# Kernel tuning notes

Measured on AMD Instinct MI355X. Metric: run time of the kernel, lower is better.

Reference implementation:

```python
import jax, jax.numpy as jnp
import numpy as np

TOP_K = 2


def setup_inputs() -> dict:
    key = jax.random.key(0)
    k0, k1, k2, k3, k4 = jax.random.split(key, 5)
    B, S, H, I, E = 4, 2048, 1024, 2816, 8
    s_h = 1.0 / np.sqrt(H)
    s_i = 1.0 / np.sqrt(I)
    return {
        "x": jax.random.normal(k0, (B, S, H), jnp.float32),
        # nn.Linear weights are stored as [out_features, in_features]
        "w_router": jax.random.normal(k1, (E, H), jnp.float32) * s_h,   # gate: H -> E
        "w_gate": jax.random.normal(k2, (E, I, H), jnp.float32) * s_h,  # per-expert gate_proj
        "w_up": jax.random.normal(k3, (E, I, H), jnp.float32) * s_h,    # per-expert up_proj
        "w_down": jax.random.normal(k4, (E, H, I), jnp.float32) * s_i,  # per-expert down_proj
    }


def reference(x, w_router, w_gate, w_up, w_down):
    B, S, H = x.shape
    E = w_router.shape[0]
    xf = x.reshape(-1, H)                      # [T, H], T = B*S

    # --- Router: softmax over experts, top-k, renormalize weights ---
    logits = jnp.einsum("th,eh->te", xf, w_router)        # [T, E]
    probs = jax.nn.softmax(logits, axis=-1)
    topw, topi = jax.lax.top_k(probs, TOP_K)              # [T, k]
    topw = topw / jnp.sum(topw, axis=-1, keepdims=True)

    # Per-token combine weight for each expert: sum_k w[t,k] * 1[idx[t,k]==e]
    onehot = (topi[..., None] == jnp.arange(E)).astype(x.dtype)  # [T, k, E]
    combine = jnp.einsum("tk,tke->te", topw, onehot)             # [T, E]

    # --- Experts: SwiGLU MLP per expert on all tokens, masked combine ---
    # (masked-dense in the original == gather-compute mathematically,
    # since silu(0)*0 = 0 and the projections have no bias)
    gate = jax.nn.silu(jnp.einsum("th,eih->eti", xf, w_gate))    # [E, T, I]
    up = jnp.einsum("th,eih->eti", xf, w_up)                     # [E, T, I]
    down = jnp.einsum("eti,ehi->eth", gate * up, w_down)         # [E, T, H]

    out = jnp.einsum("eth,te->th", down, combine)                # [T, H]
    return out.reshape(B, S, H)
```

## Files before the change

kernel.cpp:

```cpp
#include <hip/hip_runtime.h>

#define TT 8192
#define HD 1024
#define ID 2816
#define NE 8
#define NID2 (2*ID)

typedef __attribute__((ext_vector_type(8))) short short8;
typedef __attribute__((ext_vector_type(4))) float f32x4;

#define WS_TOP2I 0
#define WS_TOP2W 65536
#define WS_CNT   131072
#define WS_OFF   131136
#define WS_CUR   131200
#define WS_TMAP  131328
#define WS_SLOTW 196864
#define WS_T2S   262400
#define WS_XB    1048576ULL
#define WS_WGU   (WS_XB  + 16777216ULL)
#define WS_WDB   (WS_WGU + 92274688ULL)
#define WS_ACT   (WS_WDB + 46137344ULL)

__device__ __forceinline__ unsigned int pack_bf2(float lo, float hi) {
  unsigned int ul = __builtin_bit_cast(unsigned int, lo) + 0x8000u;
  unsigned int uh = __builtin_bit_cast(unsigned int, hi) + 0x8000u;
  return (uh & 0xffff0000u) | (ul >> 16);
}

__device__ __forceinline__ unsigned short f2bf(float f) {
  unsigned int u = __builtin_bit_cast(unsigned int, f);
  return (unsigned short)((u + 0x8000u) >> 16);
}

__device__ __forceinline__ void gload16(const void* g, void* l) {
  __builtin_amdgcn_global_load_lds(
      (const __attribute__((address_space(1))) unsigned int*)g,
      (__attribute__((address_space(3))) unsigned int*)l, 16, 0, 0);
}

__global__ __launch_bounds__(256) void router_kernel(
    const float* __restrict__ x, const float* __restrict__ wr,
    int* __restrict__ top2i, float* __restrict__ top2w,
    unsigned short* __restrict__ xb)
{
  int tid  = threadIdx.x;
  int lane = tid & 63;
  int t    = blockIdx.x * 4 + (tid >> 6);

  const float4* xp = (const float4*)(x + (size_t)t * HD + lane * 16);
  float4 xv[4];
  #pragma unroll
  for (int j = 0; j < 4; ++j) xv[j] = xp[j];

  uint4 v0, v1;
  v0.x = pack_bf2(xv[0].x, xv[0].y); v0.y = pack_bf2(xv[0].z, xv[0].w);
  v0.z = pack_bf2(xv[1].x, xv[1].y); v0.w = pack_bf2(xv[1].z, xv[1].w);
  v1.x = pack_bf2(xv[2].x, xv[2].y); v1.y = pack_bf2(xv[2].z, xv[2].w);
  v1.z = pack_bf2(xv[3].x, xv[3].y); v1.w = pack_bf2(xv[3].z, xv[3].w);
  uint4* xrow = (uint4*)(xb + (size_t)t * HD + lane * 16);
  xrow[0] = v0; xrow[1] = v1;

  float acc[NE];
  #pragma unroll
  for (int e = 0; e < NE; ++e) {
    const float4* wp = (const float4*)(wr + (size_t)e * HD + lane * 16);
    float s = 0.f;
    #pragma unroll
    for (int j = 0; j < 4; ++j) {
      float4 w = wp[j];
      s += xv[j].x * w.x + xv[j].y * w.y + xv[j].z * w.z + xv[j].w * w.w;
    }
    acc[e] = s;
  }
  #pragma unroll
  for (int d = 1; d < 64; d <<= 1) {
    #pragma unroll
    for (int e = 0; e < NE; ++e) acc[e] += __shfl_xor(acc[e], d, 64);
  }
  int   i0 = 0; float m0 = acc[0];
  #pragma unroll
  for (int e = 1; e < NE; ++e) if (acc[e] > m0) { m0 = acc[e]; i0 = e; }
  int   i1 = -1; float m1 = -3.4e38f;
  #pragma unroll
  for (int e = 0; e < NE; ++e) if (e != i0 && acc[e] > m1) { m1 = acc[e]; i1 = e; }

  float e1 = __expf(m1 - m0);
  float w0 = 1.f / (1.f + e1);
  float w1 = e1 * w0;

  if (lane == 0) {
    top2i[2 * t] = i0;  top2i[2 * t + 1] = i1;
    top2w[2 * t] = w0;  top2w[2 * t + 1] = w1;
  }
}

__global__ __launch_bounds__(256) void count_scan_kernel(
    const int* __restrict__ top2i,
    int* __restrict__ counts, int* __restrict__ offsets, int* __restrict__ cursors)
{
  __shared__ int s_cnt[NE];
  int tid = threadIdx.x;
  if (tid < NE) s_cnt[tid] = 0;
  __syncthreads();

  int c0=0,c1=0,c2=0,c3=0,c4=0,c5=0,c6=0,c7=0;
  for (int t = tid; t < TT; t += 256) {
    int e0 = top2i[2 * t], e1 = top2i[2 * t + 1];
    c0 += __popcll(__ballot(e0 == 0)) + __popcll(__ballot(e1 == 0));
    c1 += __popcll(__ballot(e0 == 1)) + __popcll(__ballot(e1 == 1));
    c2 += __popcll(__ballot(e0 == 2)) + __popcll(__ballot(e1 == 2));
    c3 += __popcll(__ballot(e0 == 3)) + __popcll(__ballot(e1 == 3));
    c4 += __popcll(__ballot(e0 == 4)) + __popcll(__ballot(e1 == 4));
    c5 += __popcll(__ballot(e0 == 5)) + __popcll(__ballot(e1 == 5));
    c6 += __popcll(__ballot(e0 == 6)) + __popcll(__ballot(e1 == 6));
    c7 += __popcll(__ballot(e0 == 7)) + __popcll(__ballot(e1 == 7));
  }
  if ((tid & 63) == 0) {
    atomicAdd(&s_cnt[0], c0); atomicAdd(&s_cnt[1], c1);
    atomicAdd(&s_cnt[2], c2); atomicAdd(&s_cnt[3], c3);
    atomicAdd(&s_cnt[4], c4); atomicAdd(&s_cnt[5], c5);
    atomicAdd(&s_cnt[6], c6); atomicAdd(&s_cnt[7], c7);
  }
  __syncthreads();
  if (tid == 0) {
    int run = 0;
    #pragma unroll
    for (int e = 0; e < NE; ++e) {
      counts[e] = s_cnt[e]; offsets[e] = run; cursors[e] = run; run += s_cnt[e];
    }
    offsets[NE] = run;
  }
}

__global__ __launch_bounds__(256) void place_kernel(
    const int* __restrict__ top2i, const float* __restrict__ top2w,
    int* __restrict__ cursors,
    int* __restrict__ token_map, float* __restrict__ slot_w, int* __restrict__ tok2slot)
{
  int tid  = threadIdx.x;
  int lane = tid & 63;
  int t    = blockIdx.x * 256 + tid;

  #pragma unroll
  for (int k = 0; k < 2; ++k) {
    int   e = top2i[2 * t + k];
    float w = top2w[2 * t + k];
    #pragma unroll
    for (int ee = 0; ee < NE; ++ee) {
      unsigned long long m = __ballot(e == ee);
      if (e == ee) {
        int leader = __ffsll((long long)m) - 1;
        int pre    = __popcll(m & ((1ull << lane) - 1ull));
        int base   = 0;
        if (lane == leader) base = atomicAdd(&cursors[ee], (int)__popcll(m));
        base = __shfl(base, leader, 64);
        token_map[base + pre] = t;
        slot_w[base + pre]    = w;
        tok2slot[2 * t + k]   = base + pre;
      }
    }
  }
}

__global__ __launch_bounds__(256) void cvt_wgu_kernel(
    const float* __restrict__ wg, const float* __restrict__ wu,
    unsigned short* __restrict__ wgu)
{
  int e    = blockIdx.y;
  int idx  = blockIdx.x * 256 + threadIdx.x;
  int col8 = idx & 127;
  int rr   = idx >> 7;
  int blk  = rr >> 7;
  int win  = rr & 127;
  const float* srow = (win < 64)
      ? wg + ((size_t)e * ID + blk * 64 + win) * HD
      : wu + ((size_t)e * ID + blk * 64 + (win - 64)) * HD;
  const float4* p = (const float4*)(srow + col8 * 8);
  float4 a = p[0], b = p[1];
  uint4 v;
  v.x = pack_bf2(a.x, a.y); v.y = pack_bf2(a.z, a.w);
  v.z = pack_bf2(b.x, b.y); v.w = pack_bf2(b.z, b.w);
  *(uint4*)(wgu + ((size_t)e * NID2 + rr) * HD + col8 * 8) = v;
}

__global__ __launch_bounds__(256) void cvt_bf16_kernel(
    const float* __restrict__ in, unsigned short* __restrict__ out, int n8)
{
  int i = blockIdx.x * 256 + threadIdx.x;
  if (i >= n8) return;
  const float4* p = (const float4*)(in + (size_t)i * 8);
  float4 a = p[0], b = p[1];
  uint4 v;
  v.x = pack_bf2(a.x, a.y); v.y = pack_bf2(a.z, a.w);
  v.z = pack_bf2(b.x, b.y); v.w = pack_bf2(b.z, b.w);
  ((uint4*)out)[i] = v;
}


#define STG(kt) { \
    size_t k1 = (size_t)((kt) * 64); \
    char* db = ldsc + (unsigned)tid * 16; \
    _Pragma("unroll") for (int c = 0; c < 4; ++c) { \
      gload16(aS[c] + k1, db + c * 4096); \
      gload16(bS[c] + k1, db + 16384 + c * 4096); } }

#define CMP() { \
    const char* sa = ldsc; \
    const char* sb = ldsc + 16384; \
    _Pragma("unroll") for (int kk = 0; kk < 2; ++kk) { \
      int kb = kk * 64 + kq; \
      short8 af[4], bfr[4]; \
      _Pragma("unroll") for (int n = 0; n < 4; ++n) \
        bfr[n] = *(const short8*)(sb + (wcn * 64 + n * 16 + arow) * 128 + (kb ^ rxor)); \
      _Pragma("unroll") for (int m = 0; m < 4; ++m) \
        af[m] = *(const short8*)(sa + (wr * 64 + m * 16 + arow) * 128 + (kb ^ rxor)); \
      __builtin_amdgcn_s_setprio(1); \
      _Pragma("unroll") for (int m = 0; m < 4; ++m) \
        _Pragma("unroll") for (int n = 0; n < 4; ++n) \
          acc[m][n] = __builtin_amdgcn_mfma_f32_16x16x32_bf16(af[m], bfr[n], acc[m][n], 0, 0, 0); \
      __builtin_amdgcn_s_setprio(0); \
    } }

#define KLOOP(NT) { \
    for (int kt = 0; kt < (NT); ++kt) { \
      if (kt) __syncthreads(); \
      STG(kt); \
      __syncthreads(); \
      CMP(); \
    } }

#define XCD_DECODE(NX, NY) \
  int nwg  = (NX) * (NY) * NE; \
  int flat = blockIdx.x + (NX) * (blockIdx.y + (NY) * blockIdx.z); \
  int qq   = nwg >> 3; \
  int wg   = (flat & 7) * qq + (flat >> 3); \
  int bx   = wg % (NX); \
  int rem  = wg / (NX); \
  int y    = rem % (NY); \
  int e    = rem / (NY);

__global__ __launch_bounds__(256, 2) void gemm1_fast(
    const unsigned short* __restrict__ xb, const unsigned short* __restrict__ wgu,
    const int* __restrict__ counts, const int* __restrict__ offsets,
    const int* __restrict__ token_map, unsigned short* __restrict__ act)
{
  __shared__ __align__(16) char smem[32768];
  char* ldsc = smem;

  XCD_DECODE(16, 44)
  int cnt = counts[e];
  int off = offsets[e];

  int tid  = threadIdx.x;
  int lane = tid & 63;
  int w    = tid >> 6;
  int wr   = w >> 1;
  int wcn  = w & 1;

  int sr8  = tid >> 3;
  int colE = (((tid & 7) ^ (sr8 & 7)) << 3);
  int rxor = (lane & 7) << 4;
  int arow = lane & 15;
  int kq   = (lane >> 4) << 4;
  int prow = (lane >> 4) << 2;

  for (int t0 = bx * 128; t0 < cnt; t0 += 2048) {
    const unsigned short* aS[4];
    const unsigned short* bS[4];
    #pragma unroll
    for (int c = 0; c < 4; ++c) {
      int rowA = t0 + c * 32 + sr8;
      int slot = off + (rowA < cnt ? rowA : cnt - 1);
      aS[c] = xb  + (size_t)token_map[slot] * HD + colE;
      bS[c] = wgu + ((size_t)e * NID2 + (size_t)y * 128 + c * 32 + sr8) * HD + colE;
    }

    f32x4 zf = {0.f, 0.f, 0.f, 0.f};
    f32x4 acc[4][4];
    #pragma unroll
    for (int m = 0; m < 4; ++m)
      #pragma unroll
      for (int n = 0; n < 4; ++n) acc[m][n] = zf;

    KLOOP(HD / 64);

    __syncthreads();
    float* xch = (float*)smem;
    if (wcn == 1) {
      float* base = xch + wr * 4096;
      #pragma unroll
      for (int m = 0; m < 4; ++m)
        #pragma unroll
        for (int n = 0; n < 4; ++n)
          #pragma unroll
          for (int r = 0; r < 4; ++r)
            base[(m * 16 + prow + r) * 64 + n * 16 + arow] = acc[m][n][r];
    }
    __syncthreads();
    if (wcn == 0) {
      const float* base = xch + wr * 4096;
      #pragma unroll
      for (int m = 0; m < 4; ++m) {
        #pragma unroll
        for (int r = 0; r < 4; ++r) {
          int row = wr * 64 + m * 16 + prow + r;
          int tr2 = t0 + row;
          if (tr2 >= cnt) continue;
          size_t ob = (size_t)(off + tr2) * ID + (size_t)y * 64 + arow;
          #pragma unroll
          for (int n = 0; n < 4; ++n) {
            float g = acc[m][n][r];
            float u = base[(m * 16 + prow + r) * 64 + n * 16 + arow];
            float h = g * u / (1.f + __expf(-g));
            act[ob + n * 16] = f2bf(h);
          }
        }
      }
    }
    __syncthreads();
  }
}

__global__ __launch_bounds__(256, 2) void gemm2_fast(
    const unsigned short* __restrict__ act, const unsigned short* __restrict__ wdb,
    const int* __restrict__ counts, const int* __restrict__ offsets,
    float* __restrict__ down)
{
  __shared__ __align__(16) char smem[32768];
  char* ldsc = smem;

  XCD_DECODE(16, 8)
  int cnt = counts[e];
  int off = offsets[e];

  int tid  = threadIdx.x;
  int lane = tid & 63;
  int w    = tid >> 6;
  int wr   = w >> 1;
  int wcn  = w & 1;

  int sr8  = tid >> 3;
  int colE = (((tid & 7) ^ (sr8 & 7)) << 3);
  int rxor = (lane & 7) << 4;
  int arow = lane & 15;
  int kq   = (lane >> 4) << 4;
  int prow = (lane >> 4) << 2;

  for (int t0 = bx * 128; t0 < cnt; t0 += 2048) {
    const unsigned short* aS[4];
    const unsigned short* bS[4];
    #pragma unroll
    for (int c = 0; c < 4; ++c) {
      int rowA = t0 + c * 32 + sr8;
      int slot = off + (rowA < cnt ? rowA : cnt - 1);
      aS[c] = act + (size_t)slot * ID + colE;
      bS[c] = wdb + ((size_t)e * HD + (size_t)y * 128 + c * 32 + sr8) * ID + colE;
    }

    f32x4 zf = {0.f, 0.f, 0.f, 0.f};
    f32x4 acc[4][4];
    #pragma unroll
    for (int m = 0; m < 4; ++m)
      #pragma unroll
      for (int n = 0; n < 4; ++n) acc[m][n] = zf;

    KLOOP(ID / 64);

    #pragma unroll
    for (int m = 0; m < 4; ++m) {
      #pragma unroll
      for (int r = 0; r < 4; ++r) {
        int row = wr * 64 + m * 16 + prow + r;
        int tr2 = t0 + row;
        if (tr2 >= cnt) continue;
        float* ob = down + (size_t)(off + tr2) * HD + (size_t)y * 128 + wcn * 64 + arow;
        #pragma unroll
        for (int n = 0; n < 4; ++n)
          ob[n * 16] = acc[m][n][r];
      }
    }
    __syncthreads();
  }
}

__global__ __launch_bounds__(256) void combine_kernel(
    const float* __restrict__ down, const float* __restrict__ slot_w,
    const int* __restrict__ tok2slot, float* __restrict__ out)
{
  int t   = blockIdx.x;
  int tid = threadIdx.x;
  int s0  = tok2slot[2 * t], s1 = tok2slot[2 * t + 1];
  float w0 = slot_w[s0], w1 = slot_w[s1];
  const float4* d0 = (const float4*)(down + (size_t)s0 * HD) + tid;
  const float4* d1 = (const float4*)(down + (size_t)s1 * HD) + tid;
  float4 a = *d0, b = *d1;
  float4 o;
  o.x = w0 * a.x + w1 * b.x;  o.y = w0 * a.y + w1 * b.y;
  o.z = w0 * a.z + w1 * b.z;  o.w = w0 * a.w + w1 * b.w;
  ((float4*)(out + (size_t)t * HD))[tid] = o;
}

extern "C" void kernel_launch(void* const* d_in, const int* in_sizes, int n_in,
                              void* d_out, int out_size, void* d_ws, size_t ws_size,
                              hipStream_t stream) {
  const float* x        = (const float*)d_in[0];
  const float* w_router = (const float*)d_in[1];
  const float* w_gate   = (const float*)d_in[2];
  const float* w_up     = (const float*)d_in[3];
  const float* w_down   = (const float*)d_in[4];

  char* ws = (char*)d_ws;
  int*   top2i    = (int*)(ws + WS_TOP2I);
  float* top2w    = (float*)(ws + WS_TOP2W);
  int*   counts   = (int*)(ws + WS_CNT);
  int*   offsets  = (int*)(ws + WS_OFF);
  int*   cursors  = (int*)(ws + WS_CUR);
  int*   tmap     = (int*)(ws + WS_TMAP);
  float* slotw    = (float*)(ws + WS_SLOTW);
  int*   tok2slot = (int*)(ws + WS_T2S);
  unsigned short* xb  = (unsigned short*)(ws + WS_XB);
  unsigned short* wgu = (unsigned short*)(ws + WS_WGU);
  unsigned short* wdb = (unsigned short*)(ws + WS_WDB);
  unsigned short* act = (unsigned short*)(ws + WS_ACT);
  float*          down = (float*)(ws + WS_WGU);

  router_kernel<<<TT / 4, 256, 0, stream>>>(x, w_router, top2i, top2w, xb);
  count_scan_kernel<<<1, 256, 0, stream>>>(top2i, counts, offsets, cursors);
  place_kernel<<<TT / 256, 256, 0, stream>>>(top2i, top2w, cursors, tmap, slotw, tok2slot);
  cvt_wgu_kernel<<<dim3(2816, NE), 256, 0, stream>>>(w_gate, w_up, wgu);
  cvt_bf16_kernel<<<11264, 256, 0, stream>>>(w_down, wdb, NE * HD * ID / 8);

  gemm1_fast<<<dim3(16, 44, NE), 256, 0, stream>>>(xb, wgu, counts, offsets, tmap, act);
  gemm2_fast<<<dim3(16, 8, NE), 256, 0, stream>>>(act, wdb, counts, offsets, down);
  combine_kernel<<<TT, 256, 0, stream>>>(down, slotw, tok2slot, (float*)d_out);
}
```

Measured before the change: 593.0 us.

## Interleave gate/up rows at 16-row granularity and enlarge down-proj GEMM tile

The fused gate/up weight is now interleaved in 16-row chunks, so each wave holds matching gate and up columns in its own accumulators. This removes the LDS exchange and extra barriers in the gemm1 SwiGLU epilogue. gemm2 moves to 512-thread blocks with a 256x256 tile, 128 KB of double-buffered dynamic LDS and 8x4 MFMA tiles per wave, to raise arithmetic intensity. The risks are higher register pressure, lower occupancy, and fewer blocks across the grid.

```diff
diff --git a/kernel.cpp b/kernel.cpp
--- a/kernel.cpp
+++ b/kernel.cpp
@@ -171,11 +171,11 @@
   int idx  = blockIdx.x * 256 + threadIdx.x;
   int col8 = idx & 127;
   int rr   = idx >> 7;
-  int blk  = rr >> 7;
-  int win  = rr & 127;
-  const float* srow = (win < 64)
-      ? wg + ((size_t)e * ID + blk * 64 + win) * HD
-      : wu + ((size_t)e * ID + blk * 64 + (win - 64)) * HD;
+  int blk  = rr >> 5;
+  int win  = rr & 31;
+  const float* srow = (win < 16)
+      ? wg + ((size_t)e * ID + blk * 16 + win) * HD
+      : wu + ((size_t)e * ID + blk * 16 + (win - 16)) * HD;
   const float4* p = (const float4*)(srow + col8 * 8);
   float4 a = p[0], b = p[1];
   uint4 v;
@@ -285,88 +285,6 @@
 
     KLOOP(HD / 64);
 
-    __syncthreads();
-    float* xch = (float*)smem;
-    if (wcn == 1) {
-      float* base = xch + wr * 4096;
-      #pragma unroll
-      for (int m = 0; m < 4; ++m)
-        #pragma unroll
-        for (int n = 0; n < 4; ++n)
-          #pragma unroll
-          for (int r = 0; r < 4; ++r)
-            base[(m * 16 + prow + r) * 64 + n * 16 + arow] = acc[m][n][r];
-    }
-    __syncthreads();
-    if (wcn == 0) {
-      const float* base = xch + wr * 4096;
-      #pragma unroll
-      for (int m = 0; m < 4; ++m) {
-        #pragma unroll
-        for (int r = 0; r < 4; ++r) {
-          int row = wr * 64 + m * 16 + prow + r;
-          int tr2 = t0 + row;
-          if (tr2 >= cnt) continue;
-          size_t ob = (size_t)(off + tr2) * ID + (size_t)y * 64 + arow;
-          #pragma unroll
-          for (int n = 0; n < 4; ++n) {
-            float g = acc[m][n][r];
-            float u = base[(m * 16 + prow + r) * 64 + n * 16 + arow];
-            float h = g * u / (1.f + __expf(-g));
-            act[ob + n * 16] = f2bf(h);
-          }
-        }
-      }
-    }
-    __syncthreads();
-  }
-}
-
-__global__ __launch_bounds__(256, 2) void gemm2_fast(
-    const unsigned short* __restrict__ act, const unsigned short* __restrict__ wdb,
-    const int* __restrict__ counts, const int* __restrict__ offsets,
-    float* __restrict__ down)
-{
-  __shared__ __align__(16) char smem[32768];
-  char* ldsc = smem;
-
-  XCD_DECODE(16, 8)
-  int cnt = counts[e];
-  int off = offsets[e];
-
-  int tid  = threadIdx.x;
-  int lane = tid & 63;
-  int w    = tid >> 6;
-  int wr   = w >> 1;
-  int wcn  = w & 1;
-
-  int sr8  = tid >> 3;
-  int colE = (((tid & 7) ^ (sr8 & 7)) << 3);
-  int rxor = (lane & 7) << 4;
-  int arow = lane & 15;
-  int kq   = (lane >> 4) << 4;
-  int prow = (lane >> 4) << 2;
-
-  for (int t0 = bx * 128; t0 < cnt; t0 += 2048) {
-    const unsigned short* aS[4];
-    const unsigned short* bS[4];
-    #pragma unroll
-    for (int c = 0; c < 4; ++c) {
-      int rowA = t0 + c * 32 + sr8;
-      int slot = off + (rowA < cnt ? rowA : cnt - 1);
-      aS[c] = act + (size_t)slot * ID + colE;
-      bS[c] = wdb + ((size_t)e * HD + (size_t)y * 128 + c * 32 + sr8) * ID + colE;
-    }
-
-    f32x4 zf = {0.f, 0.f, 0.f, 0.f};
-    f32x4 acc[4][4];
-    #pragma unroll
-    for (int m = 0; m < 4; ++m)
-      #pragma unroll
-      for (int n = 0; n < 4; ++n) acc[m][n] = zf;
-
-    KLOOP(ID / 64);
-
     #pragma unroll
     for (int m = 0; m < 4; ++m) {
       #pragma unroll
@@ -374,7 +292,106 @@
         int row = wr * 64 + m * 16 + prow + r;
         int tr2 = t0 + row;
         if (tr2 >= cnt) continue;
-        float* ob = down + (size_t)(off + tr2) * HD + (size_t)y * 128 + wcn * 64 + arow;
+        size_t ob = (size_t)(off + tr2) * ID + (size_t)y * 64 + wcn * 32 + arow;
+        #pragma unroll
+        for (int p = 0; p < 2; ++p) {
+          float g = acc[m][2 * p][r];
+          float u = acc[m][2 * p + 1][r];
+          float h = g * u / (1.f + __expf(-g));
+          act[ob + p * 16] = f2bf(h);
+        }
+      }
+    }
+    __syncthreads();
+  }
+}
+
+
+#define STG2(t) { \
+    size_t k1 = (size_t)((t) * 64); \
+    char* db = ldsc + (((t) & 1) ? 65536u : 0u) + (unsigned)tid * 16; \
+    gload16(aS[0] + k1, db);           gload16(aS[1] + k1, db + 8192); \
+    gload16(aS[2] + k1, db + 16384);   gload16(aS[3] + k1, db + 24576); \
+    gload16(bS[0] + k1, db + 32768);   gload16(bS[1] + k1, db + 40960); \
+    gload16(bS[2] + k1, db + 49152);   gload16(bS[3] + k1, db + 57344); }
+
+#define KBODY2(t, NKT) { \
+    if ((t) + 1 < (NKT)) STG2((t) + 1); \
+    const char* sa = ldsc + (((t) & 1) ? 65536u : 0u); \
+    const char* sb = sa + 32768; \
+    _Pragma("unroll") for (int kk = 0; kk < 2; ++kk) { \
+      int kb = kk * 64 + kq; \
+      short8 bfr[4], af[8]; \
+      _Pragma("unroll") for (int n = 0; n < 4; ++n) \
+        bfr[n] = *(const short8*)(sb + (wc * 64 + n * 16 + arow) * 128 + (kb ^ rxor)); \
+      _Pragma("unroll") for (int m = 0; m < 8; ++m) \
+        af[m] = *(const short8*)(sa + (wr * 128 + m * 16 + arow) * 128 + (kb ^ rxor)); \
+      __builtin_amdgcn_s_setprio(1); \
+      _Pragma("unroll") for (int m = 0; m < 8; ++m) \
+        _Pragma("unroll") for (int n = 0; n < 4; ++n) \
+          acc[m][n] = __builtin_amdgcn_mfma_f32_16x16x32_bf16(af[m], bfr[n], acc[m][n], 0, 0, 0); \
+      __builtin_amdgcn_s_setprio(0); \
+    } \
+    asm volatile("s_waitcnt vmcnt(0)" ::: "memory"); \
+    __builtin_amdgcn_s_barrier(); }
+
+__global__ __launch_bounds__(512, 2) void gemm2_fast(
+    const unsigned short* __restrict__ act, const unsigned short* __restrict__ wdb,
+    const int* __restrict__ counts, const int* __restrict__ offsets,
+    float* __restrict__ down)
+{
+  extern __shared__ char smem2[];
+  char* ldsc = smem2;
+
+  XCD_DECODE(16, 4)
+  int cnt = counts[e];
+  int off = offsets[e];
+
+  int tid  = threadIdx.x;
+  int lane = tid & 63;
+  int w    = tid >> 6;
+  int wr   = w >> 2;
+  int wc   = w & 3;
+
+  int srow0 = tid >> 3;
+  int colE  = (((tid & 7) ^ ((tid >> 3) & 7)) << 3);
+  int rxor  = (lane & 7) << 4;
+  int arow  = lane & 15;
+  int kq    = (lane >> 4) << 4;
+  int prow  = (lane >> 4) << 2;
+
+  for (int t0 = bx * 256; t0 < cnt; t0 += 4096) {
+    const unsigned short* aS[4];
+    const unsigned short* bS[4];
+    #pragma unroll
+    for (int j = 0; j < 4; ++j) {
+      int row  = srow0 + 64 * j;
+      int tr   = t0 + row;
+      int slot = off + (tr < cnt ? tr : cnt - 1);
+      aS[j] = act + (size_t)slot * ID + colE;
+      bS[j] = wdb + ((size_t)e * HD + (size_t)y * 256 + row) * ID + colE;
+    }
+
+    f32x4 zf = {0.f, 0.f, 0.f, 0.f};
+    f32x4 acc[8][4];
+    #pragma unroll
+    for (int m = 0; m < 8; ++m)
+      #pragma unroll
+      for (int n = 0; n < 4; ++n) acc[m][n] = zf;
+
+    STG2(0);
+    asm volatile("s_waitcnt vmcnt(0)" ::: "memory");
+    __builtin_amdgcn_s_barrier();
+    for (int t = 0; t < ID / 64; ++t) KBODY2(t, ID / 64);
+
+    #pragma unroll
+    for (int m = 0; m < 8; ++m) {
+      #pragma unroll
+      for (int r = 0; r < 4; ++r) {
+        int row = wr * 128 + m * 16 + prow + r;
+        int tr2 = t0 + row;
+        if (tr2 >= cnt) continue;
+        float* ob = down + (size_t)(off + tr2) * HD + (size_t)y * 256 + wc * 64 + arow;
         #pragma unroll
         for (int n = 0; n < 4; ++n)
           ob[n * 16] = acc[m][n][r];
@@ -425,6 +442,9 @@
   unsigned short* act = (unsigned short*)(ws + WS_ACT);
   float*          down = (float*)(ws + WS_WGU);
 
+  hipFuncSetAttribute((const void*)gemm2_fast,
+                      hipFuncAttributeMaxDynamicSharedMemorySize, 131072);
+
   router_kernel<<<TT / 4, 256, 0, stream>>>(x, w_router, top2i, top2w, xb);
   count_scan_kernel<<<1, 256, 0, stream>>>(top2i, counts, offsets, cursors);
   place_kernel<<<TT / 256, 256, 0, stream>>>(top2i, top2w, cursors, tmap, slotw, tok2slot);
@@ -432,6 +452,6 @@
   cvt_bf16_kernel<<<11264, 256, 0, stream>>>(w_down, wdb, NE * HD * ID / 8);
 
   gemm1_fast<<<dim3(16, 44, NE), 256, 0, stream>>>(xb, wgu, counts, offsets, tmap, act);
-  gemm2_fast<<<dim3(16, 8, NE), 256, 0, stream>>>(act, wdb, counts, offsets, down);
+  gemm2_fast<<<dim3(16, 4, NE), 512, 131072, stream>>>(act, wdb, counts, offsets, down);
   combine_kernel<<<TT, 256, 0, stream>>>(down, slotw, tok2slot, (float*)d_out);
 }
```

Measured after the change: 541.7 us. 1.09x faster.
